# Optimization experiments

Measured on AMD Instinct MI355X. Metric: run time of the kernel, lower is better.

Reference implementation:

```python
import jax, jax.numpy as jnp
import numpy as np

DIM = 256
HID = 512  # max(dim, hidden_dim)
N_SLOTS = 8
ITERS = 3
EPS = 1e-8
LN_EPS = 1e-5  # torch LayerNorm default
SCALE = DIM ** -0.5


def _ln(x, g, b):
    m = jnp.mean(x, axis=-1, keepdims=True)
    v = jnp.mean(jnp.square(x - m), axis=-1, keepdims=True)
    return (x - m) * jax.lax.rsqrt(v + LN_EPS) * g + b


def setup_inputs() -> dict:
    key = jax.random.key(0)
    ks = jax.random.split(key, 16)
    s = lambda fan_in: 1.0 / np.sqrt(fan_in)
    inp = {
        "inputs": jax.random.normal(ks[0], (64, 4096, DIM), jnp.float32),
        "slots_init": jax.random.normal(ks[1], (64, N_SLOTS, DIM), jnp.float32),
        "slots_mu": jax.random.normal(ks[2], (1, 1, DIM), jnp.float32),
        "slots_sigma": jax.random.normal(ks[3], (1, 1, DIM), jnp.float32),
        "wq": jax.random.uniform(ks[4], (DIM, DIM), jnp.float32, -s(DIM), s(DIM)),
        "bq": jnp.zeros((DIM,), jnp.float32),
        "wk": jax.random.uniform(ks[5], (DIM, DIM), jnp.float32, -s(DIM), s(DIM)),
        "bk": jnp.zeros((DIM,), jnp.float32),
        "wv": jax.random.uniform(ks[6], (DIM, DIM), jnp.float32, -s(DIM), s(DIM)),
        "bv": jnp.zeros((DIM,), jnp.float32),
        "w_ih": jax.random.uniform(ks[7], (3 * DIM, DIM), jnp.float32, -s(DIM), s(DIM)),
        "b_ih": jax.random.uniform(ks[8], (3 * DIM,), jnp.float32, -s(DIM), s(DIM)),
        "w_hh": jax.random.uniform(ks[9], (3 * DIM, DIM), jnp.float32, -s(DIM), s(DIM)),
        "b_hh": jax.random.uniform(ks[10], (3 * DIM,), jnp.float32, -s(DIM), s(DIM)),
        "mlp_w1": jax.random.uniform(ks[11], (HID, DIM), jnp.float32, -s(DIM), s(DIM)),
        "mlp_b1": jnp.zeros((HID,), jnp.float32),
        "mlp_w2": jax.random.uniform(ks[12], (DIM, HID), jnp.float32, -s(HID), s(HID)),
        "mlp_b2": jnp.zeros((DIM,), jnp.float32),
        "ln_in_g": jnp.ones((DIM,), jnp.float32),
        "ln_in_b": jnp.zeros((DIM,), jnp.float32),
        "ln_slots_g": jnp.ones((DIM,), jnp.float32),
        "ln_slots_b": jnp.zeros((DIM,), jnp.float32),
        "ln_ff_g": jnp.ones((DIM,), jnp.float32),
        "ln_ff_b": jnp.zeros((DIM,), jnp.float32),
    }
    return inp


def _gru_cell(x, h, w_ih, b_ih, w_hh, b_hh):
    # torch.nn.GRUCell: gates ordered (r, z, n)
    gi = x @ w_ih.T + b_ih  # [b, s, 3d]
    gh = h @ w_hh.T + b_hh
    i_r, i_z, i_n = jnp.split(gi, 3, axis=-1)
    h_r, h_z, h_n = jnp.split(gh, 3, axis=-1)
    r = jax.nn.sigmoid(i_r + h_r)
    z = jax.nn.sigmoid(i_z + h_z)
    n = jnp.tanh(i_n + r * h_n)
    return (1.0 - z) * n + z * h


def reference(inputs, slots_init, slots_mu, slots_sigma, wq, bq, wk, bk, wv, bv,
              w_ih, b_ih, w_hh, b_hh, mlp_w1, mlp_b1, mlp_w2, mlp_b2,
              ln_in_g, ln_in_b, ln_slots_g, ln_slots_b, ln_ff_g, ln_ff_b):
    x = _ln(inputs, ln_in_g, ln_in_b)           # [b, n, d]
    k = x @ wk.T + bk
    v = x @ wv.T + bv
    slots = slots_mu + slots_sigma * slots_init  # [b, s, d]
    for _ in range(ITERS):
        slots_prev = slots
        q = _ln(slots, ln_slots_g, ln_slots_b) @ wq.T + bq
        dots = jnp.einsum('bid,bjd->bij', q, k) * SCALE  # [b, s, n]
        attn = jax.nn.softmax(dots, axis=1) + EPS        # softmax over slots
        attn = attn / jnp.sum(attn, axis=-1, keepdims=True)
        updates = jnp.einsum('bij,bjd->bid', attn, v)    # [b, s, d]
        slots = _gru_cell(updates, slots_prev, w_ih, b_ih, w_hh, b_hh)
        h = jax.nn.relu(_ln(slots, ln_ff_g, ln_ff_b) @ mlp_w1.T + mlp_b1)
        slots = slots + (h @ mlp_w2.T + mlp_b2)
    return slots
```

## Files before the change

kernel.cpp:

```cpp
#include <hip/hip_runtime.h>
#include <hip/hip_bf16.h>

#define B_ 64
#define N_ 4096
#define D_ 256
#define S_ 8
#define HID_ 512
#define NCH_ 16

typedef __attribute__((ext_vector_type(8))) short short8;
typedef __attribute__((ext_vector_type(4))) float f32x4;

__device__ inline unsigned int f2bf(float f){
  unsigned int x = __builtin_bit_cast(unsigned int, f);
  unsigned int r = x + 0x7fffu + ((x >> 16) & 1u);
  return (r >> 16);
}
__device__ inline float bf2f(unsigned int u){
  unsigned int x = (u & 0xffffu) << 16;
  return __builtin_bit_cast(float, x);
}
__device__ inline void fma8(short8 w8, const float* xp, float& a){
#pragma unroll
  for (int e = 0; e < 8; ++e) a += bf2f((unsigned)(unsigned short)w8[e]) * xp[e];
}

__global__ __launch_bounds__(256) void kLN(const float* __restrict__ xin,
    const float* __restrict__ lng, const float* __restrict__ lnb,
    unsigned short* __restrict__ xh)
{
  const int t = threadIdx.x;
  const int wv = t >> 6, lane = t & 63;
  const float4 g4 = *(const float4*)(lng + lane * 4);
  const float4 b4 = *(const float4*)(lnb + lane * 4);
#pragma unroll 2
  for (int it = 0; it < 32; ++it){
    const long r = (long)it * 8192 + blockIdx.x * 4 + wv;
    float4 f = *(const float4*)(xin + r * 256 + lane * 4);
    float s  = f.x + f.y + f.z + f.w;
    float ss = f.x*f.x + f.y*f.y + f.z*f.z + f.w*f.w;
#pragma unroll
    for (int o = 1; o < 64; o <<= 1){ s += __shfl_xor(s, o); ss += __shfl_xor(ss, o); }
    const float mean = s * (1.f/256.f);
    const float rstd = rsqrtf(ss * (1.f/256.f) - mean * mean + 1e-5f);
    unsigned p0 = f2bf((f.x - mean)*rstd*g4.x + b4.x) | (f2bf((f.y - mean)*rstd*g4.y + b4.y) << 16);
    unsigned p1 = f2bf((f.z - mean)*rstd*g4.z + b4.z) | (f2bf((f.w - mean)*rstd*g4.w + b4.w) << 16);
    uint2 pk; pk.x = p0; pk.y = p1;
    *(uint2*)(xh + r * 256 + lane * 4) = pk;
  }
}

__global__ __launch_bounds__(256) void kPre(
    const float* __restrict__ wq, const float* __restrict__ bq,
    const float* __restrict__ wk, const float* __restrict__ bk,
    const float* __restrict__ wv, const float* __restrict__ bv,
    const float* __restrict__ wih, const float* __restrict__ bih,
    float* __restrict__ Mb, float* __restrict__ cb,
    float* __restrict__ v1b, float* __restrict__ c0b,
    float* __restrict__ bih2,
    unsigned short* __restrict__ Mbh, unsigned short* __restrict__ Wih2h)
{
  const int blk = blockIdx.x, t = threadIdx.x;
  if (blk < 256){
    const int d = blk;
    float acc = 0.f, accc = 0.f;
    for (int e = 0; e < 256; ++e){
      float wkd = wk[e*256 + d];
      acc  += wkd * wq[e*256 + t];
      accc += wkd * bq[e];
    }
    Mb[d*256 + t] = acc;
    Mbh[d*256 + t] = (unsigned short)f2bf(acc);
    if (t == 0) cb[d] = accc;
  } else if (blk < 1024){
    const int g = blk - 256;
    float acc = 0.f, accb = 0.f;
    for (int d = 0; d < 256; ++d){
      float wg = wih[g*256 + d];
      acc  += wg * wv[d*256 + t];
      accb += wg * bv[d];
    }
    Wih2h[g*256 + t] = (unsigned short)f2bf(acc);
    if (t == 0) bih2[g] = bih[g] + accb;
  } else {
    float acc = 0.f, acc0 = 0.f;
    for (int e = 0; e < 256; ++e){
      float bke = bk[e];
      acc  += wq[e*256 + t] * bke;
      acc0 += bq[e] * bke;
    }
    v1b[t] = acc;
    if (t == 0) c0b[0] = acc0;
  }
}

__global__ __launch_bounds__(256) void kCvt(
    const float* __restrict__ w_hh, const float* __restrict__ w1,
    const float* __restrict__ w2,
    unsigned short* __restrict__ whhh, unsigned short* __restrict__ w1h,
    unsigned short* __restrict__ w2h)
{
  const int i = blockIdx.x * 256 + threadIdx.x;
  if (i < 196608) whhh[i] = (unsigned short)f2bf(w_hh[i]);
  else if (i < 327680) w1h[i - 196608] = (unsigned short)f2bf(w1[i - 196608]);
  else w2h[i - 327680] = (unsigned short)f2bf(w2[i - 327680]);
}

__global__ __launch_bounds__(256) void kI(const float* __restrict__ init,
    const float* __restrict__ mu, const float* __restrict__ sig,
    const float* __restrict__ lsg, const float* __restrict__ lsb,
    const float* __restrict__ Mb, const float* __restrict__ cb,
    const float* __restrict__ v1b, const float* __restrict__ c0b,
    float* __restrict__ slots, float* __restrict__ qt, float* __restrict__ dbuf)
{
  const int b = blockIdx.x, t = threadIdx.x;
  __shared__ float xs[S_ * D_];
  __shared__ float red[4 * S_ * 2];
  __shared__ float redd[4 * S_];
  float sv[S_];
  const float muv = mu[t], sgv = sig[t];
#pragma unroll
  for (int i = 0; i < S_; ++i){
    float x = muv + sgv * init[(b*S_ + i)*D_ + t];
    sv[i] = x;
    slots[(b*S_ + i)*D_ + t] = x;
  }
  float s[S_], qq[S_];
#pragma unroll
  for (int i = 0; i < S_; ++i){ s[i] = sv[i]; qq[i] = sv[i]*sv[i]; }
#pragma unroll
  for (int o = 1; o < 64; o <<= 1){
#pragma unroll
    for (int i = 0; i < S_; ++i){ s[i] += __shfl_xor(s[i], o); qq[i] += __shfl_xor(qq[i], o); }
  }
  const int wv_ = t >> 6;
  if ((t & 63) == 0){
#pragma unroll
    for (int i = 0; i < S_; ++i){ red[(wv_*S_ + i)*2] = s[i]; red[(wv_*S_ + i)*2 + 1] = qq[i]; }
  }
  __syncthreads();
  const float g_ = lsg[t], bv_ = lsb[t];
#pragma unroll
  for (int i = 0; i < S_; ++i){
    float S0 = 0.f, Q0 = 0.f;
#pragma unroll
    for (int w2 = 0; w2 < 4; ++w2){ S0 += red[(w2*S_ + i)*2]; Q0 += red[(w2*S_ + i)*2 + 1]; }
    float mean = S0 * (1.f/256.f), var = Q0 * (1.f/256.f) - mean*mean;
    float rstd = rsqrtf(var + 1e-5f);
    xs[i*D_ + t] = (sv[i] - mean) * rstd * g_ + bv_;
  }
  __syncthreads();
  {
    const float v1v = v1b[t];
    float pd[S_];
#pragma unroll
    for (int i = 0; i < S_; ++i) pd[i] = xs[i*D_ + t] * v1v;
#pragma unroll
    for (int o = 1; o < 64; o <<= 1)
#pragma unroll
      for (int i = 0; i < S_; ++i) pd[i] += __shfl_xor(pd[i], o);
    if ((t & 63) == 0){
#pragma unroll
      for (int i = 0; i < S_; ++i) redd[wv_*S_ + i] = pd[i];
    }
    __syncthreads();
    if (t < S_) dbuf[b*S_ + t] = redd[t] + redd[S_ + t] + redd[2*S_ + t] + redd[3*S_ + t] + c0b[0];
  }
  const float4* wr = (const float4*)(Mb + (long)t * D_);
  float acc[S_];
#pragma unroll
  for (int i = 0; i < S_; ++i) acc[i] = 0.f;
  for (int kc = 0; kc < 64; ++kc){
    float4 wf = wr[kc];
#pragma unroll
    for (int i = 0; i < S_; ++i){
      float4 xf = *(const float4*)(xs + i*D_ + kc*4);
      acc[i] += wf.x*xf.x + wf.y*xf.y + wf.z*xf.z + wf.w*xf.w;
    }
  }
  const float cbv = cb[t];
#pragma unroll
  for (int i = 0; i < S_; ++i) qt[(b*S_ + i)*D_ + t] = acc[i] + cbv;
}

__global__ __launch_bounds__(256) void kD(const unsigned short* __restrict__ xh,
    const float* __restrict__ qt, const float* __restrict__ dbuf,
    float* __restrict__ numP, float* __restrict__ denP)
{
  const int b = blockIdx.y, ch = blockIdx.x, t = threadIdx.x;
  __shared__ __align__(16) char smem[4 * 64 * 37 * 4];
  __shared__ __align__(16) float sw[128 * 8];
  unsigned short* qs = (unsigned short*)smem;
  float* redbuf = (float*)smem;
  const int lane = t & 63, w = t >> 6;
  const int lr = lane & 15, lg = lane >> 4;
  const int oct = lane & 31, sh = lane >> 5;

  {
    const int rowq = t >> 4, segq = t & 15;
    uint4 z0 = {0,0,0,0}, z1 = {0,0,0,0};
    if (rowq < 8){
      const float* qr = qt + ((long)b * S_ + rowq) * D_ + segq * 16;
      float4 f0 = ((const float4*)qr)[0], f1 = ((const float4*)qr)[1];
      float4 f2 = ((const float4*)qr)[2], f3 = ((const float4*)qr)[3];
      z0.x = f2bf(f0.x)|(f2bf(f0.y)<<16); z0.y = f2bf(f0.z)|(f2bf(f0.w)<<16);
      z0.z = f2bf(f1.x)|(f2bf(f1.y)<<16); z0.w = f2bf(f1.z)|(f2bf(f1.w)<<16);
      z1.x = f2bf(f2.x)|(f2bf(f2.y)<<16); z1.y = f2bf(f2.z)|(f2bf(f2.w)<<16);
      z1.z = f2bf(f3.x)|(f2bf(f3.y)<<16); z1.w = f2bf(f3.z)|(f2bf(f3.w)<<16);
    }
    *(uint4*)(qs + rowq*264 + segq*16) = z0;
    *(uint4*)(qs + rowq*264 + segq*16 + 8) = z1;
  }
  __syncthreads();

  short8 bqf[8];
#pragma unroll
  for (int ks = 0; ks < 8; ++ks)
    bqf[ks] = *(const short8*)(qs + lr*264 + ks*32 + lg*8);
  __syncthreads();

  const float dd = (lr < 8) ? dbuf[b*S_ + lr] * 0.0625f : 0.f;

  float acc4[4][8];
#pragma unroll
  for (int s = 0; s < 4; ++s)
#pragma unroll
    for (int e = 0; e < 8; ++e) acc4[s][e] = 0.f;
  float den4[4] = {0.f, 0.f, 0.f, 0.f};

  for (int ph = 0; ph < 2; ++ph){
    const long j0 = (long)ch * 256 + ph * 128;
#pragma unroll
    for (int tau = 0; tau < 2; ++tau){
      const long jt = j0 + w*32 + tau*16;
      const unsigned short* kr = xh + ((long)b * N_ + jt + lr) * 256;
      f32x4 d = {0,0,0,0};
#pragma unroll
      for (int ks = 0; ks < 8; ++ks){
        short8 afk = *(const short8*)(kr + ks*32 + lg*8);
        d = __builtin_amdgcn_mfma_f32_16x16x32_bf16(afk, bqf[ks], d, 0, 0, 0);
      }
#pragma unroll
      for (int r = 0; r < 4; ++r){
        float x = d[r] * 0.0625f + dd;
        float m = x;
        m = fmaxf(m, __shfl_xor(m, 1));
        m = fmaxf(m, __shfl_xor(m, 2));
        m = fmaxf(m, __shfl_xor(m, 4));
        float e = __expf(x - m);
        float ssum = e;
        ssum += __shfl_xor(ssum, 1);
        ssum += __shfl_xor(ssum, 2);
        ssum += __shfl_xor(ssum, 4);
        float wv = e / ssum + 1e-8f;
        if (lr < 8) sw[(w*32 + tau*16 + lg*4 + r)*8 + lr] = wv;
      }
    }
    const unsigned short* vrow = xh + ((long)b * N_ + j0 + w*32) * 256 + oct*8;
    const float* swr = sw + (w*32)*8 + sh*4;
#pragma unroll 4
    for (int j = 0; j < 32; ++j){
      uint4 v = *(const uint4*)(vrow + (long)j * 256);
      float4 w4 = *(const float4*)(swr + j*8);
      float xv[8];
      xv[0] = bf2f(v.x); xv[1] = bf2f(v.x >> 16);
      xv[2] = bf2f(v.y); xv[3] = bf2f(v.y >> 16);
      xv[4] = bf2f(v.z); xv[5] = bf2f(v.z >> 16);
      xv[6] = bf2f(v.w); xv[7] = bf2f(v.w >> 16);
#pragma unroll
      for (int e = 0; e < 8; ++e){
        acc4[0][e] += w4.x * xv[e];
        acc4[1][e] += w4.y * xv[e];
        acc4[2][e] += w4.z * xv[e];
        acc4[3][e] += w4.w * xv[e];
      }
      den4[0] += w4.x; den4[1] += w4.y; den4[2] += w4.z; den4[3] += w4.w;
    }
  }

  __syncthreads();
  {
    float* myred = redbuf + (w*64 + lane)*37;
#pragma unroll
    for (int s = 0; s < 4; ++s){
#pragma unroll
      for (int e = 0; e < 8; ++e) myred[s*8 + e] = acc4[s][e];
      myred[32 + s] = den4[s];
    }
  }
  __syncthreads();
  {
    const int i_ = t >> 5, oo = t & 31;
    const int ssh = i_ >> 2, ss = i_ & 3;
    float outv[8] = {0,0,0,0,0,0,0,0};
    float den = 0.f;
#pragma unroll
    for (int wv2 = 0; wv2 < 4; ++wv2){
      const float* p = redbuf + (wv2*64 + ssh*32 + oo)*37;
#pragma unroll
      for (int e = 0; e < 8; ++e) outv[e] += p[ss*8 + e];
      den += p[32 + ss];
    }
    float* numC = numP + ((((long)ch * B_ + b) * S_ + i_) * D_) + oo * 8;
    float4 a0 = {outv[0], outv[1], outv[2], outv[3]};
    float4 a1 = {outv[4], outv[5], outv[6], outv[7]};
    *(float4*)(numC) = a0;
    *(float4*)(numC + 4) = a1;
    if (oo == 0) denP[((long)b * S_ + i_) * NCH_ + ch] = den;
  }
}

__device__ inline void stats2(const float v[2], float* red, int t, float* mean, float* rstd){
  float s[2], q2[2];
#pragma unroll
  for (int ii = 0; ii < 2; ++ii){ s[ii] = v[ii]; q2[ii] = v[ii]*v[ii]; }
#pragma unroll
  for (int o = 1; o < 64; o <<= 1){
#pragma unroll
    for (int ii = 0; ii < 2; ++ii){ s[ii] += __shfl_xor(s[ii], o); q2[ii] += __shfl_xor(q2[ii], o); }
  }
  const int wv = t >> 6;
  if ((t & 63) == 0){
#pragma unroll
    for (int ii = 0; ii < 2; ++ii){ red[(wv*2 + ii)*2] = s[ii]; red[(wv*2 + ii)*2 + 1] = q2[ii]; }
  }
  __syncthreads();
#pragma unroll
  for (int ii = 0; ii < 2; ++ii){
    float S0 = 0.f, Q0 = 0.f;
#pragma unroll
    for (int w2 = 0; w2 < 4; ++w2){ S0 += red[(w2*2 + ii)*2]; Q0 += red[(w2*2 + ii)*2 + 1]; }
    float m = S0 * (1.f/256.f);
    float var = Q0 * (1.f/256.f) - m*m;
    mean[ii] = m; rstd[ii] = rsqrtf(var + 1e-5f);
  }
  __syncthreads();
}

__global__ __launch_bounds__(256) void kS(
    const float* __restrict__ numP, const float* __restrict__ denP,
    const float* __restrict__ slots_in,
    const unsigned short* __restrict__ Wih2h, const float* __restrict__ bih2,
    const unsigned short* __restrict__ whhh, const float* __restrict__ b_hh,
    const unsigned short* __restrict__ w1h, const float* __restrict__ b1,
    const unsigned short* __restrict__ w2h, const float* __restrict__ b2,
    const float* __restrict__ fg, const float* __restrict__ fb,
    const float* __restrict__ lsg, const float* __restrict__ lsb,
    const unsigned short* __restrict__ Mbh, const float* __restrict__ cbv,
    const float* __restrict__ v1b, const float* __restrict__ c0b,
    float* __restrict__ outp, float* __restrict__ qout, float* __restrict__ dbuf,
    int write_q)
{
  const int blk = blockIdx.x;
  const int b = blk >> 2, i0 = (blk & 3) * 2;
  const int t = threadIdx.x;
  const int grp = t >> 3, j = t & 7;
  __shared__ float us[2][D_], hs[2][D_], xs2[2][D_];
  __shared__ float gi_l[2][768], gh_l[2][768];
  __shared__ float h2s[2][HID_];
  __shared__ float o2[2][D_];
  __shared__ float red[4 * 2 * 2];
  const long base = (long)(b * S_ + i0) * D_;
#pragma unroll
  for (int ii = 0; ii < 2; ++ii){
    int si = b*S_ + i0 + ii;
    float dv = 0.f;
#pragma unroll
    for (int ch = 0; ch < NCH_; ++ch) dv += denP[(long)si * NCH_ + ch];
    float u = 0.f;
    for (int ch = 0; ch < NCH_; ++ch)
      u += numP[(((long)ch * B_ + b) * S_ + i0 + ii) * D_ + t];
    us[ii][t] = u / dv;
    hs[ii][t] = slots_in[base + ii*D_ + t];
  }
  __syncthreads();
  for (int q = 0; q < 24; ++q){
    const int gcol = grp + q * 32;
    const short8* wi = (const short8*)(Wih2h + (long)gcol * D_);
    const short8* wh = (const short8*)(whhh + (long)gcol * D_);
    float ai[2] = {0,0}, ah[2] = {0,0};
#pragma unroll
    for (int c = 0; c < 4; ++c){
      const int u = j + c*8;
      short8 wf = wi[u];
      short8 hf = wh[u];
#pragma unroll
      for (int ii = 0; ii < 2; ++ii){
        fma8(wf, &us[ii][u*8], ai[ii]);
        fma8(hf, &hs[ii][u*8], ah[ii]);
      }
    }
#pragma unroll
    for (int o = 1; o < 8; o <<= 1){
#pragma unroll
      for (int ii = 0; ii < 2; ++ii){ ai[ii] += __shfl_xor(ai[ii], o); ah[ii] += __shfl_xor(ah[ii], o); }
    }
    if (j == 0){
#pragma unroll
      for (int ii = 0; ii < 2; ++ii){ gi_l[ii][gcol] = ai[ii]; gh_l[ii][gcol] = ah[ii]; }
    }
  }
  __syncthreads();
  const float bir = bih2[t], biz = bih2[256 + t], bin_ = bih2[512 + t];
  const float bhr = b_hh[t], bhz = b_hh[256 + t], bhn = b_hh[512 + t];
  float nh[2];
#pragma unroll
  for (int ii = 0; ii < 2; ++ii){
    float r = 1.f / (1.f + __expf(-(gi_l[ii][t] + bir + gh_l[ii][t] + bhr)));
    float z = 1.f / (1.f + __expf(-(gi_l[ii][256 + t] + biz + gh_l[ii][256 + t] + bhz)));
    float n = tanhf(gi_l[ii][512 + t] + bin_ + r * (gh_l[ii][512 + t] + bhn));
    nh[ii] = (1.f - z) * n + z * hs[ii][t];
  }
  float mean[2], rstd[2];
  stats2(nh, red, t, mean, rstd);
  const float fgv = fg[t], fbv = fb[t];
#pragma unroll
  for (int ii = 0; ii < 2; ++ii) xs2[ii][t] = (nh[ii] - mean[ii]) * rstd[ii] * fgv + fbv;
  __syncthreads();
  for (int q = 0; q < 16; ++q){
    const int gcol = grp + q * 32;
    const short8* wr = (const short8*)(w1h + (long)gcol * D_);
    float a[2] = {0,0};
#pragma unroll
    for (int c = 0; c < 4; ++c){
      const int u = j + c*8;
      short8 wf = wr[u];
#pragma unroll
      for (int ii = 0; ii < 2; ++ii) fma8(wf, &xs2[ii][u*8], a[ii]);
    }
#pragma unroll
    for (int o = 1; o < 8; o <<= 1)
#pragma unroll
      for (int ii = 0; ii < 2; ++ii) a[ii] += __shfl_xor(a[ii], o);
    if (j == 0){
      float bb = b1[gcol];
#pragma unroll
      for (int ii = 0; ii < 2; ++ii) h2s[ii][gcol] = fmaxf(a[ii] + bb, 0.f);
    }
  }
  __syncthreads();
  for (int q = 0; q < 8; ++q){
    const int gcol = grp + q * 32;
    const short8* wr = (const short8*)(w2h + (long)gcol * HID_);
    float a[2] = {0,0};
#pragma unroll
    for (int c = 0; c < 8; ++c){
      const int u = j + c*8;
      short8 wf = wr[u];
#pragma unroll
      for (int ii = 0; ii < 2; ++ii) fma8(wf, &h2s[ii][u*8], a[ii]);
    }
#pragma unroll
    for (int o = 1; o < 8; o <<= 1)
#pragma unroll
      for (int ii = 0; ii < 2; ++ii) a[ii] += __shfl_xor(a[ii], o);
    if (j == 0){
#pragma unroll
      for (int ii = 0; ii < 2; ++ii) o2[ii][gcol] = a[ii];
    }
  }
  __syncthreads();
  float outv[2];
  const float b2v = b2[t];
#pragma unroll
  for (int ii = 0; ii < 2; ++ii){
    outv[ii] = nh[ii] + o2[ii][t] + b2v;
    outp[base + ii*D_ + t] = outv[ii];
  }
  if (write_q){
    float mean2[2], rstd2[2];
    stats2(outv, red, t, mean2, rstd2);
    const float lg2 = lsg[t], lb2 = lsb[t];
#pragma unroll
    for (int ii = 0; ii < 2; ++ii) xs2[ii][t] = (outv[ii] - mean2[ii]) * rstd2[ii] * lg2 + lb2;
    __syncthreads();
    {
      const float v1v = v1b[t];
      float pd[2];
#pragma unroll
      for (int ii = 0; ii < 2; ++ii) pd[ii] = xs2[ii][t] * v1v;
#pragma unroll
      for (int o = 1; o < 64; o <<= 1)
#pragma unroll
        for (int ii = 0; ii < 2; ++ii) pd[ii] += __shfl_xor(pd[ii], o);
      const int wv = t >> 6;
      if ((t & 63) == 0){ red[wv*2] = pd[0]; red[wv*2 + 1] = pd[1]; }
      __syncthreads();
      if (t < 2) dbuf[b*S_ + i0 + t] = red[t] + red[2 + t] + red[4 + t] + red[6 + t] + c0b[0];
    }
    for (int q = 0; q < 8; ++q){
      const int gcol = grp + q * 32;
      const short8* wr = (const short8*)(Mbh + (long)gcol * D_);
      float a[2] = {0,0};
#pragma unroll
      for (int c = 0; c < 4; ++c){
        const int u = j + c*8;
        short8 wf = wr[u];
#pragma unroll
        for (int ii = 0; ii < 2; ++ii) fma8(wf, &xs2[ii][u*8], a[ii]);
      }
#pragma unroll
      for (int o = 1; o < 8; o <<= 1)
#pragma unroll
        for (int ii = 0; ii < 2; ++ii) a[ii] += __shfl_xor(a[ii], o);
      if (j == 0){
        float bb = cbv[gcol];
#pragma unroll
        for (int ii = 0; ii < 2; ++ii) qout[(long)(b*S_ + i0 + ii)*D_ + gcol] = a[ii] + bb;
      }
    }
  }
}

extern "C" void kernel_launch(void* const* d_in, const int* in_sizes, int n_in,
                              void* d_out, int out_size, void* d_ws, size_t ws_size,
                              hipStream_t stream)
{
  const float* inputs     = (const float*)d_in[0];
  const float* slots_init = (const float*)d_in[1];
  const float* slots_mu   = (const float*)d_in[2];
  const float* slots_sig  = (const float*)d_in[3];
  const float* wq   = (const float*)d_in[4];
  const float* bq   = (const float*)d_in[5];
  const float* wk   = (const float*)d_in[6];
  const float* bk   = (const float*)d_in[7];
  const float* wv   = (const float*)d_in[8];
  const float* bv   = (const float*)d_in[9];
  const float* w_ih = (const float*)d_in[10];
  const float* b_ih = (const float*)d_in[11];
  const float* w_hh = (const float*)d_in[12];
  const float* b_hh = (const float*)d_in[13];
  const float* w1   = (const float*)d_in[14];
  const float* b1   = (const float*)d_in[15];
  const float* w2   = (const float*)d_in[16];
  const float* b2   = (const float*)d_in[17];
  const float* lig  = (const float*)d_in[18];
  const float* lib  = (const float*)d_in[19];
  const float* lsg  = (const float*)d_in[20];
  const float* lsb  = (const float*)d_in[21];
  const float* ffg  = (const float*)d_in[22];
  const float* ffb  = (const float*)d_in[23];
  float* out = (float*)d_out;

  char* ws = (char*)d_ws;
  float* qtb  = (float*)(ws);
  float* numP = (float*)(ws + 524288);
  float* denP = (float*)(ws + 8912896);
  float* dbuf = (float*)(ws + 8945664);
  float* Mb   = (float*)(ws + 8947712);
  float* cb   = (float*)(ws + 9209856);
  float* v1b  = (float*)(ws + 9210880);
  float* c0b  = (float*)(ws + 9211904);
  float* bih2 = (float*)(ws + 9212928);
  unsigned short* Mbh   = (unsigned short*)(ws + 9217024);
  unsigned short* Wih2h = (unsigned short*)(ws + 9348096);
  unsigned short* whhh  = (unsigned short*)(ws + 9741312);
  unsigned short* w1h   = (unsigned short*)(ws + 10134528);
  unsigned short* w2h   = (unsigned short*)(ws + 10396672);
  unsigned short* xh    = (unsigned short*)(ws + 10658816);
  float* slots = out;

  kLN<<<2048, 256, 0, stream>>>(inputs, lig, lib, xh);
  kPre<<<1025, 256, 0, stream>>>(wq, bq, wk, bk, wv, bv, w_ih, b_ih,
                                 Mb, cb, v1b, c0b, bih2, Mbh, Wih2h);
  kCvt<<<1792, 256, 0, stream>>>(w_hh, w1, w2, whhh, w1h, w2h);
  kI<<<64, 256, 0, stream>>>(slots_init, slots_mu, slots_sig, lsg, lsb,
                             Mb, cb, v1b, c0b, slots, qtb, dbuf);
  for (int it = 0; it < 3; ++it){
    kD<<<dim3(NCH_, B_), 256, 0, stream>>>(xh, qtb, dbuf, numP, denP);
    kS<<<256, 256, 0, stream>>>(numP, denP, slots, Wih2h, bih2, whhh, b_hh,
                                w1h, b1, w2h, b2, ffg, ffb, lsg, lsb,
                                Mbh, cb, v1b, c0b,
                                slots, qtb, dbuf, (it < 2) ? 1 : 0);
  }
}
```

Baseline: 411.9 us.

## Tile weight-precompute kernel and drop in-block reduction in attention kernel

The weight-fold precompute kernel now has each block compute 16 output rows, with the shared operand staged in shared memory. This cuts the grid from 1025 to 65 blocks and reuses each weight load across 16 accumulators. The attention kernel no longer reduces across its four waves through shared memory with two barriers. Each wave writes its own partial numerator and denominator, which makes 64 partials per slot, and the slot-update kernel sums all of them. This trades fewer syncs and less shared memory in the hot kernel for four times the partial-buffer traffic and longer reduction loops in the consumer.

```diff
diff --git a/kernel.cpp b/kernel.cpp
--- a/kernel.cpp
+++ b/kernel.cpp
@@ -6,7 +6,6 @@
 #define D_ 256
 #define S_ 8
 #define HID_ 512
-#define NCH_ 16
 
 typedef __attribute__((ext_vector_type(8))) short short8;
 typedef __attribute__((ext_vector_type(4))) float f32x4;
@@ -60,28 +59,65 @@
     float* __restrict__ bih2,
     unsigned short* __restrict__ Mbh, unsigned short* __restrict__ Wih2h)
 {
+  __shared__ float tile[4096];
   const int blk = blockIdx.x, t = threadIdx.x;
-  if (blk < 256){
-    const int d = blk;
-    float acc = 0.f, accc = 0.f;
+  if (blk < 16){
+    const int d0 = blk * 16;
+#pragma unroll
+    for (int r = 0; r < 16; ++r){
+      const int idx = r * 256 + t;
+      const int e = idx >> 4, dd = idx & 15;
+      tile[idx] = wk[e*256 + d0 + dd];
+    }
+    __syncthreads();
+    float acc[16], accc[16];
+#pragma unroll
+    for (int dd = 0; dd < 16; ++dd){ acc[dd] = 0.f; accc[dd] = 0.f; }
     for (int e = 0; e < 256; ++e){
-      float wkd = wk[e*256 + d];
-      acc  += wkd * wq[e*256 + t];
-      accc += wkd * bq[e];
-    }
-    Mb[d*256 + t] = acc;
-    Mbh[d*256 + t] = (unsigned short)f2bf(acc);
-    if (t == 0) cb[d] = accc;
-  } else if (blk < 1024){
-    const int g = blk - 256;
-    float acc = 0.f, accb = 0.f;
+      const float wqv = wq[e*256 + t];
+      const float bqe = bq[e];
+      const float4* kr = (const float4*)&tile[e*16];
+      float4 k0 = kr[0], k1 = kr[1], k2 = kr[2], k3 = kr[3];
+      acc[0]+=k0.x*wqv; acc[1]+=k0.y*wqv; acc[2]+=k0.z*wqv; acc[3]+=k0.w*wqv;
+      acc[4]+=k1.x*wqv; acc[5]+=k1.y*wqv; acc[6]+=k1.z*wqv; acc[7]+=k1.w*wqv;
+      acc[8]+=k2.x*wqv; acc[9]+=k2.y*wqv; acc[10]+=k2.z*wqv; acc[11]+=k2.w*wqv;
+      acc[12]+=k3.x*wqv; acc[13]+=k3.y*wqv; acc[14]+=k3.z*wqv; acc[15]+=k3.w*wqv;
+      accc[0]+=k0.x*bqe; accc[1]+=k0.y*bqe; accc[2]+=k0.z*bqe; accc[3]+=k0.w*bqe;
+      accc[4]+=k1.x*bqe; accc[5]+=k1.y*bqe; accc[6]+=k1.z*bqe; accc[7]+=k1.w*bqe;
+      accc[8]+=k2.x*bqe; accc[9]+=k2.y*bqe; accc[10]+=k2.z*bqe; accc[11]+=k2.w*bqe;
+      accc[12]+=k3.x*bqe; accc[13]+=k3.y*bqe; accc[14]+=k3.z*bqe; accc[15]+=k3.w*bqe;
+    }
+#pragma unroll
+    for (int dd = 0; dd < 16; ++dd){
+      float v = acc[dd];
+      Mb[(d0+dd)*256 + t] = v;
+      Mbh[(d0+dd)*256 + t] = (unsigned short)f2bf(v);
+    }
+#pragma unroll
+    for (int dd = 0; dd < 16; ++dd) if (t == dd) cb[d0+dd] = accc[dd];
+  } else if (blk < 64){
+    const int g0 = (blk - 16) * 16;
+#pragma unroll
+    for (int r = 0; r < 16; ++r) tile[r*256 + t] = wih[(long)(g0+r)*256 + t];
+    __syncthreads();
+    float acc[16], accb[16];
+#pragma unroll
+    for (int gg = 0; gg < 16; ++gg){ acc[gg] = 0.f; accb[gg] = 0.f; }
     for (int d = 0; d < 256; ++d){
-      float wg = wih[g*256 + d];
-      acc  += wg * wv[d*256 + t];
-      accb += wg * bv[d];
-    }
-    Wih2h[g*256 + t] = (unsigned short)f2bf(acc);
-    if (t == 0) bih2[g] = bih[g] + accb;
+      const float wvv = wv[d*256 + t];
+      const float bvd = bv[d];
+#pragma unroll
+      for (int gg = 0; gg < 16; ++gg){
+        float wg = tile[gg*256 + d];
+        acc[gg]  += wg * wvv;
+        accb[gg] += wg * bvd;
+      }
+    }
+#pragma unroll
+    for (int gg = 0; gg < 16; ++gg)
+      Wih2h[(long)(g0+gg)*256 + t] = (unsigned short)f2bf(acc[gg]);
+#pragma unroll
+    for (int gg = 0; gg < 16; ++gg) if (t == gg) bih2[g0+gg] = bih[g0+gg] + accb[gg];
   } else {
     float acc = 0.f, acc0 = 0.f;
     for (int e = 0; e < 256; ++e){
@@ -188,10 +224,8 @@
     float* __restrict__ numP, float* __restrict__ denP)
 {
   const int b = blockIdx.y, ch = blockIdx.x, t = threadIdx.x;
-  __shared__ __align__(16) char smem[4 * 64 * 37 * 4];
-  __shared__ __align__(16) float sw[128 * 8];
-  unsigned short* qs = (unsigned short*)smem;
-  float* redbuf = (float*)smem;
+  __shared__ __align__(16) unsigned short qs[16 * 264];
+  __shared__ float sw[128 * 8];
   const int lane = t & 63, w = t >> 6;
   const int lr = lane & 15, lg = lane >> 4;
   const int oct = lane & 31, sh = lane >> 5;
@@ -217,7 +251,6 @@
 #pragma unroll
   for (int ks = 0; ks < 8; ++ks)
     bqf[ks] = *(const short8*)(qs + lr*264 + ks*32 + lg*8);
-  __syncthreads();
 
   const float dd = (lr < 8) ? dbuf[b*S_ + lr] * 0.0625f : 0.f;
 
@@ -278,35 +311,20 @@
     }
   }
 
-  __syncthreads();
-  {
-    float* myred = redbuf + (w*64 + lane)*37;
-#pragma unroll
-    for (int s = 0; s < 4; ++s){
-#pragma unroll
-      for (int e = 0; e < 8; ++e) myred[s*8 + e] = acc4[s][e];
-      myred[32 + s] = den4[s];
-    }
-  }
-  __syncthreads();
-  {
-    const int i_ = t >> 5, oo = t & 31;
-    const int ssh = i_ >> 2, ss = i_ & 3;
-    float outv[8] = {0,0,0,0,0,0,0,0};
-    float den = 0.f;
-#pragma unroll
-    for (int wv2 = 0; wv2 < 4; ++wv2){
-      const float* p = redbuf + (wv2*64 + ssh*32 + oo)*37;
-#pragma unroll
-      for (int e = 0; e < 8; ++e) outv[e] += p[ss*8 + e];
-      den += p[32 + ss];
-    }
-    float* numC = numP + ((((long)ch * B_ + b) * S_ + i_) * D_) + oo * 8;
-    float4 a0 = {outv[0], outv[1], outv[2], outv[3]};
-    float4 a1 = {outv[4], outv[5], outv[6], outv[7]};
-    *(float4*)(numC) = a0;
-    *(float4*)(numC + 4) = a1;
-    if (oo == 0) denP[((long)b * S_ + i_) * NCH_ + ch] = den;
+  const int chw = ch * 4 + w;
+#pragma unroll
+  for (int s = 0; s < 4; ++s){
+    const int slot = sh*4 + s;
+    float* p = numP + (((long)chw * B_ + b) * S_ + slot) * D_ + oct*8;
+    float4 a0 = {acc4[s][0], acc4[s][1], acc4[s][2], acc4[s][3]};
+    float4 a1 = {acc4[s][4], acc4[s][5], acc4[s][6], acc4[s][7]};
+    *(float4*)(p) = a0;
+    *(float4*)(p + 4) = a1;
+  }
+  if (oct == 0){
+#pragma unroll
+    for (int s = 0; s < 4; ++s)
+      denP[((long)b * S_ + sh*4 + s) * 64 + chw] = den4[s];
   }
 }
 
@@ -365,11 +383,10 @@
   for (int ii = 0; ii < 2; ++ii){
     int si = b*S_ + i0 + ii;
     float dv = 0.f;
-#pragma unroll
-    for (int ch = 0; ch < NCH_; ++ch) dv += denP[(long)si * NCH_ + ch];
+    for (int c = 0; c < 64; ++c) dv += denP[(long)si * 64 + c];
     float u = 0.f;
-    for (int ch = 0; ch < NCH_; ++ch)
-      u += numP[(((long)ch * B_ + b) * S_ + i0 + ii) * D_ + t];
+    for (int c = 0; c < 64; ++c)
+      u += numP[(((long)c * B_ + b) * S_ + i0 + ii) * D_ + t];
     us[ii][t] = u / dv;
     hs[ii][t] = slots_in[base + ii*D_ + t];
   }
@@ -545,29 +562,29 @@
   char* ws = (char*)d_ws;
   float* qtb  = (float*)(ws);
   float* numP = (float*)(ws + 524288);
-  float* denP = (float*)(ws + 8912896);
-  float* dbuf = (float*)(ws + 8945664);
-  float* Mb   = (float*)(ws + 8947712);
-  float* cb   = (float*)(ws + 9209856);
-  float* v1b  = (float*)(ws + 9210880);
-  float* c0b  = (float*)(ws + 9211904);
-  float* bih2 = (float*)(ws + 9212928);
-  unsigned short* Mbh   = (unsigned short*)(ws + 9217024);
-  unsigned short* Wih2h = (unsigned short*)(ws + 9348096);
-  unsigned short* whhh  = (unsigned short*)(ws + 9741312);
-  unsigned short* w1h   = (unsigned short*)(ws + 10134528);
-  unsigned short* w2h   = (unsigned short*)(ws + 10396672);
-  unsigned short* xh    = (unsigned short*)(ws + 10658816);
+  float* denP = (float*)(ws + 34078720);
+  float* dbuf = (float*)(ws + 34209792);
+  float* Mb   = (float*)(ws + 34211840);
+  float* cb   = (float*)(ws + 34473984);
+  float* v1b  = (float*)(ws + 34475008);
+  float* c0b  = (float*)(ws + 34476032);
+  float* bih2 = (float*)(ws + 34477056);
+  unsigned short* Mbh   = (unsigned short*)(ws + 34481152);
+  unsigned short* Wih2h = (unsigned short*)(ws + 34612224);
+  unsigned short* whhh  = (unsigned short*)(ws + 35005440);
+  unsigned short* w1h   = (unsigned short*)(ws + 35398656);
+  unsigned short* w2h   = (unsigned short*)(ws + 35660800);
+  unsigned short* xh    = (unsigned short*)(ws + 35922944);
   float* slots = out;
 
   kLN<<<2048, 256, 0, stream>>>(inputs, lig, lib, xh);
-  kPre<<<1025, 256, 0, stream>>>(wq, bq, wk, bk, wv, bv, w_ih, b_ih,
-                                 Mb, cb, v1b, c0b, bih2, Mbh, Wih2h);
+  kPre<<<65, 256, 0, stream>>>(wq, bq, wk, bk, wv, bv, w_ih, b_ih,
+                               Mb, cb, v1b, c0b, bih2, Mbh, Wih2h);
   kCvt<<<1792, 256, 0, stream>>>(w_hh, w1, w2, whhh, w1h, w2h);
   kI<<<64, 256, 0, stream>>>(slots_init, slots_mu, slots_sig, lsg, lsb,
                              Mb, cb, v1b, c0b, slots, qtb, dbuf);
   for (int it = 0; it < 3; ++it){
-    kD<<<dim3(NCH_, B_), 256, 0, stream>>>(xh, qtb, dbuf, numP, denP);
+    kD<<<dim3(16, B_), 256, 0, stream>>>(xh, qtb, dbuf, numP, denP);
     kS<<<256, 256, 0, stream>>>(numP, denP, slots, Wih2h, bih2, whhh, b_hh,
                                 w1h, b1, w2h, b2, ffg, ffb, lsg, lsb,
                                 Mbh, cb, v1b, c0b,
```

Result: slower. 485.1 us (+17.8%).

## Tile weight-precompute matmuls in shared memory and fold weight conversion into kPre

Applied to the files above, without the earlier changes.

The weight precompute kernel now has each block compute 16 output rows, staging the wk or w_ih slice in shared memory so wq/wv rows are reused 16 times. Before, each row was its own block doing strided scalar global loads. The separate bf16 conversion kernel for w_hh, w1 and w2 is merged into the same launch, which removes one kernel launch. The cost is fewer blocks for the matmul part (64 instead of 1024), so less parallelism, and more register pressure from the 16-wide accumulators.

```diff
diff --git a/kernel.cpp b/kernel.cpp
--- a/kernel.cpp
+++ b/kernel.cpp
@@ -55,34 +55,75 @@
     const float* __restrict__ wk, const float* __restrict__ bk,
     const float* __restrict__ wv, const float* __restrict__ bv,
     const float* __restrict__ wih, const float* __restrict__ bih,
+    const float* __restrict__ w_hh, const float* __restrict__ w1,
+    const float* __restrict__ w2,
     float* __restrict__ Mb, float* __restrict__ cb,
     float* __restrict__ v1b, float* __restrict__ c0b,
     float* __restrict__ bih2,
-    unsigned short* __restrict__ Mbh, unsigned short* __restrict__ Wih2h)
+    unsigned short* __restrict__ Mbh, unsigned short* __restrict__ Wih2h,
+    unsigned short* __restrict__ whhh, unsigned short* __restrict__ w1h,
+    unsigned short* __restrict__ w2h)
 {
+  __shared__ float tile[4096];
   const int blk = blockIdx.x, t = threadIdx.x;
-  if (blk < 256){
-    const int d = blk;
-    float acc = 0.f, accc = 0.f;
+  if (blk < 16){
+    const int d0 = blk * 16;
+#pragma unroll
+    for (int r = 0; r < 16; ++r){
+      const int idx = r * 256 + t;
+      const int e = idx >> 4, dd = idx & 15;
+      tile[idx] = wk[e*256 + d0 + dd];
+    }
+    __syncthreads();
+    float acc[16], accc[16];
+#pragma unroll
+    for (int dd = 0; dd < 16; ++dd){ acc[dd] = 0.f; accc[dd] = 0.f; }
     for (int e = 0; e < 256; ++e){
-      float wkd = wk[e*256 + d];
-      acc  += wkd * wq[e*256 + t];
-      accc += wkd * bq[e];
-    }
-    Mb[d*256 + t] = acc;
-    Mbh[d*256 + t] = (unsigned short)f2bf(acc);
-    if (t == 0) cb[d] = accc;
-  } else if (blk < 1024){
-    const int g = blk - 256;
-    float acc = 0.f, accb = 0.f;
+      const float wqv = wq[e*256 + t];
+      const float bqe = bq[e];
+      const float4* kr = (const float4*)&tile[e*16];
+      float4 k0 = kr[0], k1 = kr[1], k2 = kr[2], k3 = kr[3];
+      acc[0]+=k0.x*wqv; acc[1]+=k0.y*wqv; acc[2]+=k0.z*wqv; acc[3]+=k0.w*wqv;
+      acc[4]+=k1.x*wqv; acc[5]+=k1.y*wqv; acc[6]+=k1.z*wqv; acc[7]+=k1.w*wqv;
+      acc[8]+=k2.x*wqv; acc[9]+=k2.y*wqv; acc[10]+=k2.z*wqv; acc[11]+=k2.w*wqv;
+      acc[12]+=k3.x*wqv; acc[13]+=k3.y*wqv; acc[14]+=k3.z*wqv; acc[15]+=k3.w*wqv;
+      accc[0]+=k0.x*bqe; accc[1]+=k0.y*bqe; accc[2]+=k0.z*bqe; accc[3]+=k0.w*bqe;
+      accc[4]+=k1.x*bqe; accc[5]+=k1.y*bqe; accc[6]+=k1.z*bqe; accc[7]+=k1.w*bqe;
+      accc[8]+=k2.x*bqe; accc[9]+=k2.y*bqe; accc[10]+=k2.z*bqe; accc[11]+=k2.w*bqe;
+      accc[12]+=k3.x*bqe; accc[13]+=k3.y*bqe; accc[14]+=k3.z*bqe; accc[15]+=k3.w*bqe;
+    }
+#pragma unroll
+    for (int dd = 0; dd < 16; ++dd){
+      float v = acc[dd];
+      Mb[(d0+dd)*256 + t] = v;
+      Mbh[(d0+dd)*256 + t] = (unsigned short)f2bf(v);
+    }
+#pragma unroll
+    for (int dd = 0; dd < 16; ++dd) if (t == dd) cb[d0+dd] = accc[dd];
+  } else if (blk < 64){
+    const int g0 = (blk - 16) * 16;
+#pragma unroll
+    for (int r = 0; r < 16; ++r) tile[r*256 + t] = wih[(long)(g0+r)*256 + t];
+    __syncthreads();
+    float acc[16], accb[16];
+#pragma unroll
+    for (int gg = 0; gg < 16; ++gg){ acc[gg] = 0.f; accb[gg] = 0.f; }
     for (int d = 0; d < 256; ++d){
-      float wg = wih[g*256 + d];
-      acc  += wg * wv[d*256 + t];
-      accb += wg * bv[d];
-    }
-    Wih2h[g*256 + t] = (unsigned short)f2bf(acc);
-    if (t == 0) bih2[g] = bih[g] + accb;
-  } else {
+      const float wvv = wv[d*256 + t];
+      const float bvd = bv[d];
+#pragma unroll
+      for (int gg = 0; gg < 16; ++gg){
+        float wg = tile[gg*256 + d];
+        acc[gg]  += wg * wvv;
+        accb[gg] += wg * bvd;
+      }
+    }
+#pragma unroll
+    for (int gg = 0; gg < 16; ++gg)
+      Wih2h[(long)(g0+gg)*256 + t] = (unsigned short)f2bf(acc[gg]);
+#pragma unroll
+    for (int gg = 0; gg < 16; ++gg) if (t == gg) bih2[g0+gg] = bih[g0+gg] + accb[gg];
+  } else if (blk == 64){
     float acc = 0.f, acc0 = 0.f;
     for (int e = 0; e < 256; ++e){
       float bke = bk[e];
@@ -91,19 +132,12 @@
     }
     v1b[t] = acc;
     if (t == 0) c0b[0] = acc0;
-  }
-}
-
-__global__ __launch_bounds__(256) void kCvt(
-    const float* __restrict__ w_hh, const float* __restrict__ w1,
-    const float* __restrict__ w2,
-    unsigned short* __restrict__ whhh, unsigned short* __restrict__ w1h,
-    unsigned short* __restrict__ w2h)
-{
-  const int i = blockIdx.x * 256 + threadIdx.x;
-  if (i < 196608) whhh[i] = (unsigned short)f2bf(w_hh[i]);
-  else if (i < 327680) w1h[i - 196608] = (unsigned short)f2bf(w1[i - 196608]);
-  else w2h[i - 327680] = (unsigned short)f2bf(w2[i - 327680]);
+  } else {
+    const int i = (blk - 65) * 256 + t;
+    if (i < 196608) whhh[i] = (unsigned short)f2bf(w_hh[i]);
+    else if (i < 327680) w1h[i - 196608] = (unsigned short)f2bf(w1[i - 196608]);
+    else w2h[i - 327680] = (unsigned short)f2bf(w2[i - 327680]);
+  }
 }
 
 __global__ __launch_bounds__(256) void kI(const float* __restrict__ init,
@@ -561,9 +595,10 @@
   float* slots = out;
 
   kLN<<<2048, 256, 0, stream>>>(inputs, lig, lib, xh);
-  kPre<<<1025, 256, 0, stream>>>(wq, bq, wk, bk, wv, bv, w_ih, b_ih,
-                                 Mb, cb, v1b, c0b, bih2, Mbh, Wih2h);
-  kCvt<<<1792, 256, 0, stream>>>(w_hh, w1, w2, whhh, w1h, w2h);
+  kPre<<<1857, 256, 0, stream>>>(wq, bq, wk, bk, wv, bv, w_ih, b_ih,
+                                 w_hh, w1, w2,
+                                 Mb, cb, v1b, c0b, bih2, Mbh, Wih2h,
+                                 whhh, w1h, w2h);
   kI<<<64, 256, 0, stream>>>(slots_init, slots_mu, slots_sig, lsg, lsb,
                              Mb, cb, v1b, c0b, slots, qtb, dbuf);
   for (int it = 0; it < 3; ++it){
```

Result: slower. 458.5 us (+11.3%).
